# Kernel optimization log

Measured on AMD Instinct MI355X. Metric: run time of the kernel, lower is better.

Reference implementation:

```python
import jax, jax.numpy as jnp
import numpy as np

N = 50000      # nodes
E = 640000     # edges
F_IN = 128     # input features
H = 128        # hidden = 2**7
C = 40         # classes


def setup_inputs() -> dict:
    key = jax.random.key(0)
    ks = jax.random.split(key, 10)
    x = jax.random.normal(ks[0], (N, F_IN), dtype=jnp.float32)
    edge_index = jax.random.randint(ks[1], (2, E), 0, N, dtype=jnp.int32)
    edge_weight = jax.random.uniform(ks[2], (E,), dtype=jnp.float32)
    def glorot(k, fan_in, fan_out):
        s = (6.0 / (fan_in + fan_out)) ** 0.5
        return jax.random.uniform(k, (fan_in, fan_out), jnp.float32, -s, s)
    return {
        "x": x,
        "edge_index": edge_index,
        "edge_weight": edge_weight,
        "W1": glorot(ks[3], F_IN, H), "b1": jnp.zeros((H,), jnp.float32),
        "W2": glorot(ks[4], H, H),    "b2": jnp.zeros((H,), jnp.float32),
        "W3": glorot(ks[5], H, C),    "b3": jnp.zeros((C,), jnp.float32),
    }


def gcn_conv(x, W, b, src, dst, ew, n):
    """PyG GCNConv: add self-loops, symmetric deg normalization, gather-scatter-add."""
    loop = jnp.arange(n, dtype=src.dtype)
    src_sl = jnp.concatenate([src, loop])
    dst_sl = jnp.concatenate([dst, loop])
    w_sl = jnp.concatenate([ew, jnp.ones((n,), ew.dtype)])
    deg = jax.ops.segment_sum(w_sl, dst_sl, num_segments=n)         # [N]
    dinv = jnp.where(deg > 0, jax.lax.rsqrt(deg), 0.0)
    norm = dinv[src_sl] * w_sl * dinv[dst_sl]                        # [E+N]
    h = x @ W                                                        # [N, out]
    msg = h[src_sl] * norm[:, None]                                  # gather + scale
    out = jax.ops.segment_sum(msg, dst_sl, num_segments=n)          # scatter-add
    return out + b


def reference(x, edge_index, edge_weight, W1, b1, W2, b2, W3, b3):
    # eval-mode forward: dropout and dropedge are identity (training=False)
    src, dst = edge_index[0], edge_index[1]
    n = x.shape[0]
    h = jax.nn.relu(gcn_conv(x, W1, b1, src, dst, edge_weight, n))
    h = jax.nn.relu(gcn_conv(h, W2, b2, src, dst, edge_weight, n))
    return gcn_conv(h, W3, b3, src, dst, edge_weight, n)
```

## Files before the change

### kernel.cpp

```cpp
#include <hip/hip_runtime.h>
#include <hip/hip_fp16.h>

constexpr int N_NODES = 50000;
constexpr int N_EDGES = 640000;

constexpr int NBLK  = 256;
constexpr int EPB   = N_EDGES / NBLK;
constexpr int NBUCK = (N_NODES + 255) / 256;
constexpr int GBM   = (N_NODES + 63) / 64;

typedef _Float16 half8  __attribute__((ext_vector_type(8)));
typedef _Float16 half4v __attribute__((ext_vector_type(4)));
typedef float    floatx4 __attribute__((ext_vector_type(4)));


__global__ void wconv_k(const float* __restrict__ W1, const float* __restrict__ W2,
                        const float* __restrict__ W3, _Float16* __restrict__ Wt1,
                        _Float16* __restrict__ Wt2, _Float16* __restrict__ Wt3,
                        float* __restrict__ deg) {
    int i = blockIdx.x * 256 + threadIdx.x;
    if (i < N_NODES) deg[i] = 0.f;
    if (i < 16384) {
        int n = i >> 7, k = i & 127;
        Wt1[n * 128 + k] = (_Float16)W1[k * 128 + n];
    } else if (i < 32768) {
        int j = i - 16384; int n = j >> 7, k = j & 127;
        Wt2[n * 128 + k] = (_Float16)W2[k * 128 + n];
    } else if (i < 32768 + 6144) {
        int j = i - 32768; int n = j >> 7, k = j & 127;
        Wt3[n * 128 + k] = (_Float16)((n < 40) ? W3[k * 40 + n] : 0.f);
    }
}


template<typename TIN, int F_OUT, int NT, bool FUSE_HIST>
__global__ __launch_bounds__(256) void gemm_mfma_k(const TIN* __restrict__ X,
        const _Float16* __restrict__ Wt, __half* __restrict__ H,
        const int* __restrict__ dst, int* __restrict__ gh,
        const float* __restrict__ ew, float* __restrict__ deg) {
    if constexpr (FUSE_HIST) {
        if (blockIdx.x < NBLK) {
            __shared__ int lh[256];
            int t = threadIdx.x, b = blockIdx.x;
            lh[t] = 0;
            __syncthreads();
            int e0 = b * EPB;
            for (int j = t; j < EPB; j += 256) {
                int d = dst[e0 + j];
                atomicAdd(&lh[d >> 8], 1);
                atomicAdd(&deg[d], ew[e0 + j]);
            }
            __syncthreads();
            if (t < NBUCK) gh[b * NBUCK + t] = lh[t];
            return;
        }
    }
    int bid = FUSE_HIST ? (int)blockIdx.x - NBLK : (int)blockIdx.x;

    __shared__ _Float16 Xs[64 * 136];
    int tid = threadIdx.x;
    int row0 = bid * 64;

    if constexpr (sizeof(TIN) == 4) {
        for (int idx = tid; idx < 2048; idx += 256) {
            int r = idx >> 5, c4 = idx & 31;
            float4 v = {0.f, 0.f, 0.f, 0.f};
            if (row0 + r < N_NODES)
                v = *(const float4*)((const float*)X + (size_t)(row0 + r) * 128 + c4 * 4);
            half4v h;
            h[0] = (_Float16)v.x; h[1] = (_Float16)v.y;
            h[2] = (_Float16)v.z; h[3] = (_Float16)v.w;
            *(half4v*)&Xs[r * 136 + c4 * 4] = h;
        }
    } else {
        for (int idx = tid; idx < 1024; idx += 256) {
            int r = idx >> 4, c8 = idx & 15;
            int4 v = {0, 0, 0, 0};
            if (row0 + r < N_NODES)
                v = *(const int4*)((const __half*)X + (size_t)(row0 + r) * 128 + c8 * 8);
            *(int4*)&Xs[r * 136 + c8 * 8] = v;
        }
    }
    __syncthreads();

    int lane = tid & 63;
    int wv   = tid >> 6;
    int m    = lane & 15;
    int q    = lane >> 4;

    half8 af[4];
    #pragma unroll
    for (int kt = 0; kt < 4; kt++)
        af[kt] = *(const half8*)&Xs[(wv * 16 + m) * 136 + kt * 32 + q * 8];

    floatx4 acc[NT];
    #pragma unroll
    for (int nt = 0; nt < NT; nt++) { acc[nt][0] = 0.f; acc[nt][1] = 0.f; acc[nt][2] = 0.f; acc[nt][3] = 0.f; }

    #pragma unroll
    for (int nt = 0; nt < NT; nt++) {
        const _Float16* wp = Wt + (size_t)(nt * 16 + m) * 128 + q * 8;
        half8 b0 = *(const half8*)(wp);
        half8 b1 = *(const half8*)(wp + 32);
        half8 b2 = *(const half8*)(wp + 64);
        half8 b3 = *(const half8*)(wp + 96);
        acc[nt] = __builtin_amdgcn_mfma_f32_16x16x32_f16(af[0], b0, acc[nt], 0, 0, 0);
        acc[nt] = __builtin_amdgcn_mfma_f32_16x16x32_f16(af[1], b1, acc[nt], 0, 0, 0);
        acc[nt] = __builtin_amdgcn_mfma_f32_16x16x32_f16(af[2], b2, acc[nt], 0, 0, 0);
        acc[nt] = __builtin_amdgcn_mfma_f32_16x16x32_f16(af[3], b3, acc[nt], 0, 0, 0);
    }

    #pragma unroll
    for (int nt = 0; nt < NT; nt++) {
        #pragma unroll
        for (int r = 0; r < 4; r++)
            Xs[(wv * 16 + q * 4 + r) * 136 + nt * 16 + m] = (_Float16)acc[nt][r];
    }

    if constexpr (F_OUT == 128) {
        for (int g = lane; g < 256; g += 64) {
            int r = g >> 4, c8 = g & 15;
            int row = row0 + wv * 16 + r;
            if (row < N_NODES)
                *(int4*)((__half*)H + (size_t)row * 128 + c8 * 8) =
                    *(const int4*)&Xs[(wv * 16 + r) * 136 + c8 * 8];
        }
    } else {
        for (int g = lane; g < 80; g += 64) {
            int r = g / 5, seg = g - r * 5;
            int row = row0 + wv * 16 + r;
            if (row < N_NODES)
                *(int4*)((__half*)H + (size_t)row * 40 + seg * 8) =
                    *(const int4*)&Xs[(wv * 16 + r) * 136 + seg * 8];
        }
    }
}


__global__ __launch_bounds__(256) void scan1_k(int* __restrict__ gh, int* __restrict__ total,
                                               const float* __restrict__ deg,
                                               float* __restrict__ dinv) {
    __shared__ int s[256];
    int t = threadIdx.x, b = blockIdx.x;
    int nd = b * 256 + t;
    if (nd < N_NODES) dinv[nd] = rsqrtf(1.0f + deg[nd]);
    int v = gh[t * NBUCK + b];
    s[t] = v;
    __syncthreads();
    int x = v;
    for (int off = 1; off < 256; off <<= 1) {
        int u = (t >= off) ? s[t - off] : 0;
        __syncthreads();
        x += u; s[t] = x;
        __syncthreads();
    }
    gh[t * NBUCK + b] = x - v;
    if (t == 255) total[b] = x;
}


__global__ __launch_bounds__(256) void bucket_k(const int* __restrict__ src,
        const int* __restrict__ dst, const float* __restrict__ ew,
        const int* __restrict__ gh, const int* __restrict__ total,
        int2* __restrict__ bkt) {
    __shared__ int cur[256];
    __shared__ int sc[256];
    int t = threadIdx.x, b = blockIdx.x;
    int v = (t < NBUCK) ? total[t] : 0;
    sc[t] = v;
    __syncthreads();
    int x = v;
    for (int off = 1; off < 256; off <<= 1) {
        int u = (t >= off) ? sc[t - off] : 0;
        __syncthreads();
        x += u; sc[t] = x;
        __syncthreads();
    }
    if (t < NBUCK) cur[t] = (x - v) + gh[b * NBUCK + t];
    __syncthreads();
    int e0 = b * EPB;
    for (int j = t; j < EPB; j += 256) {
        int d = dst[e0 + j];
        int pos = atomicAdd(&cur[d >> 8], 1);
        bkt[pos] = make_int2(src[e0 + j] | (d << 16), __float_as_int(ew[e0 + j]));
    }
}


__global__ __launch_bounds__(256) void final_k(const int2* __restrict__ bkt,
        const int* __restrict__ total, const float* __restrict__ dinv,
        int2* __restrict__ ev, int* __restrict__ rowptr) {
    __shared__ int   cnt[256];
    __shared__ int   s[256];
    __shared__ float dloc[256];
    int t = threadIdx.x, b = blockIdx.x;

    int nd = b * 256 + t;
    dloc[t] = (nd < N_NODES) ? dinv[nd] : 0.f;
    cnt[t] = 0;

    int v = (t < NBUCK) ? total[t] : 0;
    s[t] = v;
    __syncthreads();
    int x = v;
    for (int off = 1; off < 256; off <<= 1) {
        int u = (t >= off) ? s[t - off] : 0;
        __syncthreads();
        x += u; s[t] = x;
        __syncthreads();
    }
    int base = (b == 0) ? 0 : s[b - 1];
    int cntb = total[b];
    __syncthreads();

    for (int j = t; j < cntb; j += 256)
        atomicAdd(&cnt[(bkt[base + j].x >> 16) & 255], 1);
    __syncthreads();

    int v2 = cnt[t];
    s[t] = v2;
    __syncthreads();
    int x2 = v2;
    for (int off = 1; off < 256; off <<= 1) {
        int u = (t >= off) ? s[t - off] : 0;
        __syncthreads();
        x2 += u; s[t] = x2;
        __syncthreads();
    }
    int off_t = x2 - v2;
    if (nd < N_NODES) rowptr[nd] = base + off_t;
    if (b == 0 && t == 0) rowptr[N_NODES] = N_EDGES;
    s[t] = off_t;
    __syncthreads();

    for (int j = t; j < cntb; j += 256) {
        int2 r = bkt[base + j];
        int bin  = (r.x >> 16) & 255;
        int sidx = r.x & 0xFFFF;
        float wv = __int_as_float(r.y) * dinv[sidx] * dloc[bin];
        int p = atomicAdd(&s[bin], 1);
        ev[base + p] = make_int2(sidx, __float_as_int(wv));
    }
}


__global__ __launch_bounds__(256) void agg128_k(const __half* __restrict__ H,
        const int2* __restrict__ ev, const int* __restrict__ rowptr,
        const float* __restrict__ dinv, const float* __restrict__ bias,
        __half* __restrict__ out) {
    int lane = threadIdx.x & 63;
    int node = __builtin_amdgcn_readfirstlane(blockIdx.x * 4 + (threadIdx.x >> 6));
    if (node >= N_NODES) return;
    const __half2* __restrict__ H2 = (const __half2*)H;
    float di = dinv[node];
    float dii = di * di;
    float2 hs = __half22float2(H2[(size_t)node * 64 + lane]);
    float ax = dii * hs.x, ay = dii * hs.y;
    int e0 = rowptr[node], e1 = rowptr[node + 1];
    int e = e0;
    for (; e + 4 <= e1; e += 4) {
        int2 p0 = ev[e + 0];
        int2 p1 = ev[e + 1];
        int2 p2 = ev[e + 2];
        int2 p3 = ev[e + 3];
        float2 g0 = __half22float2(H2[(size_t)p0.x * 64 + lane]);
        float2 g1 = __half22float2(H2[(size_t)p1.x * 64 + lane]);
        float2 g2 = __half22float2(H2[(size_t)p2.x * 64 + lane]);
        float2 g3 = __half22float2(H2[(size_t)p3.x * 64 + lane]);
        float v0 = __int_as_float(p0.y);
        float v1 = __int_as_float(p1.y);
        float v2 = __int_as_float(p2.y);
        float v3 = __int_as_float(p3.y);
        ax = fmaf(v0, g0.x, ax); ay = fmaf(v0, g0.y, ay);
        ax = fmaf(v1, g1.x, ax); ay = fmaf(v1, g1.y, ay);
        ax = fmaf(v2, g2.x, ax); ay = fmaf(v2, g2.y, ay);
        ax = fmaf(v3, g3.x, ax); ay = fmaf(v3, g3.y, ay);
    }
    for (; e < e1; e++) {
        int2 p = ev[e];
        float v = __int_as_float(p.y);
        float2 g = __half22float2(H2[(size_t)p.x * 64 + lane]);
        ax = fmaf(v, g.x, ax);
        ay = fmaf(v, g.y, ay);
    }
    float2 b = *(const float2*)&bias[2 * lane];
    ax = fmaxf(ax + b.x, 0.f);
    ay = fmaxf(ay + b.y, 0.f);
    ((__half2*)out)[(size_t)node * 64 + lane] = __float22half2_rn(make_float2(ax, ay));
}


__global__ __launch_bounds__(256) void agg40_k(const __half* __restrict__ Y,
        const int2* __restrict__ ev, const int* __restrict__ rowptr,
        const float* __restrict__ dinv, const float* __restrict__ bias,
        float* __restrict__ out) {
    int lane = threadIdx.x & 63;
    int node = __builtin_amdgcn_readfirstlane(blockIdx.x * 4 + (threadIdx.x >> 6));
    if (node >= N_NODES) return;
    const __half2* __restrict__ Y2 = (const __half2*)Y;
    int h = lane >> 5;
    int l = lane & 31;
    int f = (l < 20) ? l : 0;
    float di = dinv[node];
    float dii = di * di;
    float ax = 0.f, ay = 0.f;
    if (h == 0) {
        float2 ys = __half22float2(Y2[(size_t)node * 20 + f]);
        ax = dii * ys.x; ay = dii * ys.y;
    }
    int e0 = rowptr[node], e1 = rowptr[node + 1];
    int e = e0;
    for (; e + 4 <= e1; e += 4) {
        int2 p0 = ev[e + h * 2 + 0];
        int2 p1 = ev[e + h * 2 + 1];
        float2 g0 = __half22float2(Y2[(size_t)p0.x * 20 + f]);
        float2 g1 = __half22float2(Y2[(size_t)p1.x * 20 + f]);
        float v0 = __int_as_float(p0.y);
        float v1 = __int_as_float(p1.y);
        ax = fmaf(v0, g0.x, ax); ay = fmaf(v0, g0.y, ay);
        ax = fmaf(v1, g1.x, ax); ay = fmaf(v1, g1.y, ay);
    }
    for (int ee = e + h; ee < e1; ee += 2) {
        int2 p = ev[ee];
        float v = __int_as_float(p.y);
        float2 g = __half22float2(Y2[(size_t)p.x * 20 + f]);
        ax = fmaf(v, g.x, ax);
        ay = fmaf(v, g.y, ay);
    }
    ax += __shfl_xor(ax, 32);
    ay += __shfl_xor(ay, 32);
    if (lane < 20) {
        float2 b = *(const float2*)&bias[2 * lane];
        float2 o;
        o.x = ax + b.x;
        o.y = ay + b.y;
        *(float2*)&out[(size_t)node * 40 + 2 * lane] = o;
    }
}


extern "C" void kernel_launch(void* const* d_in, const int* in_sizes, int n_in,
                              void* d_out, int out_size, void* d_ws, size_t ws_size,
                              hipStream_t stream) {
    const float* x  = (const float*)d_in[0];
    const int*   ei = (const int*)d_in[1];
    const int*   src = ei;
    const int*   dst = ei + N_EDGES;
    const float* ew = (const float*)d_in[2];
    const float* W1 = (const float*)d_in[3];
    const float* b1 = (const float*)d_in[4];
    const float* W2 = (const float*)d_in[5];
    const float* b2 = (const float*)d_in[6];
    const float* W3 = (const float*)d_in[7];
    const float* b3 = (const float*)d_in[8];
    float* out = (float*)d_out;

    char* w = (char*)d_ws;
    auto alloc = [&](size_t bytes) {
        char* p = w;
        w += (bytes + 255) & ~(size_t)255;
        return p;
    };
    float*     dinv   = (float*)    alloc((size_t)N_NODES * 4);
    float*     deg    = (float*)    alloc((size_t)N_NODES * 4);
    int*       rowptr = (int*)      alloc((size_t)(N_NODES + 1) * 4);
    int*       gh     = (int*)      alloc((size_t)NBLK * NBUCK * 4);
    int*       total  = (int*)      alloc((size_t)NBUCK * 4);
    int2*      bkt    = (int2*)     alloc((size_t)N_EDGES * 8);
    int2*      ev     = (int2*)     alloc((size_t)N_EDGES * 8);
    __half*    hbuf   = (__half*)   alloc((size_t)N_NODES * 128 * 2);
    __half*    abuf   = (__half*)   alloc((size_t)N_NODES * 128 * 2);
    __half*    ybuf   = (__half*)   alloc((size_t)N_NODES * 40 * 2);
    _Float16*  Wt1    = (_Float16*) alloc((size_t)128 * 128 * 2);
    _Float16*  Wt2    = (_Float16*) alloc((size_t)128 * 128 * 2);
    _Float16*  Wt3    = (_Float16*) alloc((size_t)48 * 128 * 2);

    constexpr int GA = (N_NODES + 3) / 4;

    wconv_k<<<196, 256, 0, stream>>>(W1, W2, W3, Wt1, Wt2, Wt3, deg);
    gemm_mfma_k<float, 128, 8, true><<<NBLK + GBM, 256, 0, stream>>>(x, Wt1, hbuf, dst, gh, ew, deg);
    scan1_k<<<NBUCK, 256, 0, stream>>>(gh, total, deg, dinv);
    bucket_k<<<NBLK, 256, 0, stream>>>(src, dst, ew, gh, total, bkt);
    final_k<<<NBUCK, 256, 0, stream>>>(bkt, total, dinv, ev, rowptr);

    agg128_k<<<GA, 256, 0, stream>>>(hbuf, ev, rowptr, dinv, b1, abuf);
    gemm_mfma_k<__half, 128, 8, false><<<GBM, 256, 0, stream>>>(abuf, Wt2, hbuf, nullptr, nullptr, nullptr, nullptr);
    agg128_k<<<GA, 256, 0, stream>>>(hbuf, ev, rowptr, dinv, b2, abuf);
    gemm_mfma_k<__half, 40, 3, false><<<GBM, 256, 0, stream>>>(abuf, Wt3, ybuf, nullptr, nullptr, nullptr, nullptr);
    agg40_k<<<GA, 256, 0, stream>>>(ybuf, ev, rowptr, dinv, b3, out);
}
```

Measured before the change: 268.8 us.

## Compute degrees in final_k and defer source-side normalization to first aggregation

Degree accumulation moves out of the histogram pass, which used global float atomics on deg, and into final_k as per-bucket shared-memory atomic sums, which also write dinv. Because dinv of source nodes is not yet known when final_k writes edge values, the first 128-wide aggregation multiplies each edge weight by dinv[src] and writes the normalized value back into ev for later layers. This removes global atomics and the deg buffer and its zeroing. In exchange, the first aggregation pays extra dinv gathers and scattered writes to ev.

Measured after the change: 257.0 us. 1.05x faster.

```diff
diff --git a/kernel.cpp b/kernel.cpp
--- a/kernel.cpp
+++ b/kernel.cpp
@@ -16,10 +16,8 @@
 
 __global__ void wconv_k(const float* __restrict__ W1, const float* __restrict__ W2,
                         const float* __restrict__ W3, _Float16* __restrict__ Wt1,
-                        _Float16* __restrict__ Wt2, _Float16* __restrict__ Wt3,
-                        float* __restrict__ deg) {
+                        _Float16* __restrict__ Wt2, _Float16* __restrict__ Wt3) {
     int i = blockIdx.x * 256 + threadIdx.x;
-    if (i < N_NODES) deg[i] = 0.f;
     if (i < 16384) {
         int n = i >> 7, k = i & 127;
         Wt1[n * 128 + k] = (_Float16)W1[k * 128 + n];
@@ -36,8 +34,7 @@
 template<typename TIN, int F_OUT, int NT, bool FUSE_HIST>
 __global__ __launch_bounds__(256) void gemm_mfma_k(const TIN* __restrict__ X,
         const _Float16* __restrict__ Wt, __half* __restrict__ H,
-        const int* __restrict__ dst, int* __restrict__ gh,
-        const float* __restrict__ ew, float* __restrict__ deg) {
+        const int* __restrict__ dst, int* __restrict__ gh) {
     if constexpr (FUSE_HIST) {
         if (blockIdx.x < NBLK) {
             __shared__ int lh[256];
@@ -45,11 +42,8 @@
             lh[t] = 0;
             __syncthreads();
             int e0 = b * EPB;
-            for (int j = t; j < EPB; j += 256) {
-                int d = dst[e0 + j];
-                atomicAdd(&lh[d >> 8], 1);
-                atomicAdd(&deg[d], ew[e0 + j]);
-            }
+            for (int j = t; j < EPB; j += 256)
+                atomicAdd(&lh[dst[e0 + j] >> 8], 1);
             __syncthreads();
             if (t < NBUCK) gh[b * NBUCK + t] = lh[t];
             return;
@@ -137,13 +131,9 @@
 }
 
 
-__global__ __launch_bounds__(256) void scan1_k(int* __restrict__ gh, int* __restrict__ total,
-                                               const float* __restrict__ deg,
-                                               float* __restrict__ dinv) {
+__global__ __launch_bounds__(256) void scan1_k(int* __restrict__ gh, int* __restrict__ total) {
     __shared__ int s[256];
     int t = threadIdx.x, b = blockIdx.x;
-    int nd = b * 256 + t;
-    if (nd < N_NODES) dinv[nd] = rsqrtf(1.0f + deg[nd]);
     int v = gh[t * NBUCK + b];
     s[t] = v;
     __syncthreads();
@@ -188,16 +178,14 @@
 
 
 __global__ __launch_bounds__(256) void final_k(const int2* __restrict__ bkt,
-        const int* __restrict__ total, const float* __restrict__ dinv,
-        int2* __restrict__ ev, int* __restrict__ rowptr) {
+        const int* __restrict__ total, int2* __restrict__ ev,
+        int* __restrict__ rowptr, float* __restrict__ dinv) {
     __shared__ int   cnt[256];
+    __shared__ float wsum[256];
     __shared__ int   s[256];
-    __shared__ float dloc[256];
     int t = threadIdx.x, b = blockIdx.x;
 
-    int nd = b * 256 + t;
-    dloc[t] = (nd < N_NODES) ? dinv[nd] : 0.f;
-    cnt[t] = 0;
+    cnt[t] = 0; wsum[t] = 0.f;
 
     int v = (t < NBUCK) ? total[t] : 0;
     s[t] = v;
@@ -213,8 +201,12 @@
     int cntb = total[b];
     __syncthreads();
 
-    for (int j = t; j < cntb; j += 256)
-        atomicAdd(&cnt[(bkt[base + j].x >> 16) & 255], 1);
+    for (int j = t; j < cntb; j += 256) {
+        int2 r = bkt[base + j];
+        int bin = (r.x >> 16) & 255;
+        atomicAdd(&cnt[bin], 1);
+        atomicAdd(&wsum[bin], __int_as_float(r.y));
+    }
     __syncthreads();
 
     int v2 = cnt[t];
@@ -228,8 +220,14 @@
         __syncthreads();
     }
     int off_t = x2 - v2;
-    if (nd < N_NODES) rowptr[nd] = base + off_t;
+    int nd = b * 256 + t;
+    float dv = rsqrtf(1.0f + wsum[t]);
+    if (nd < N_NODES) {
+        rowptr[nd] = base + off_t;
+        dinv[nd]   = dv;
+    }
     if (b == 0 && t == 0) rowptr[N_NODES] = N_EDGES;
+    wsum[t] = dv;
     s[t] = off_t;
     __syncthreads();
 
@@ -237,15 +235,16 @@
         int2 r = bkt[base + j];
         int bin  = (r.x >> 16) & 255;
         int sidx = r.x & 0xFFFF;
-        float wv = __int_as_float(r.y) * dinv[sidx] * dloc[bin];
+        float wv = __int_as_float(r.y) * wsum[bin];
         int p = atomicAdd(&s[bin], 1);
         ev[base + p] = make_int2(sidx, __float_as_int(wv));
     }
 }
 
 
+template<bool PREMUL>
 __global__ __launch_bounds__(256) void agg128_k(const __half* __restrict__ H,
-        const int2* __restrict__ ev, const int* __restrict__ rowptr,
+        int2* __restrict__ ev, const int* __restrict__ rowptr,
         const float* __restrict__ dinv, const float* __restrict__ bias,
         __half* __restrict__ out) {
     int lane = threadIdx.x & 63;
@@ -263,14 +262,24 @@
         int2 p1 = ev[e + 1];
         int2 p2 = ev[e + 2];
         int2 p3 = ev[e + 3];
+        float v0 = __int_as_float(p0.y);
+        float v1 = __int_as_float(p1.y);
+        float v2 = __int_as_float(p2.y);
+        float v3 = __int_as_float(p3.y);
+        if constexpr (PREMUL) {
+            v0 *= dinv[p0.x]; v1 *= dinv[p1.x];
+            v2 *= dinv[p2.x]; v3 *= dinv[p3.x];
+            if (lane == 0) {
+                ev[e + 0].y = __float_as_int(v0);
+                ev[e + 1].y = __float_as_int(v1);
+                ev[e + 2].y = __float_as_int(v2);
+                ev[e + 3].y = __float_as_int(v3);
+            }
+        }
         float2 g0 = __half22float2(H2[(size_t)p0.x * 64 + lane]);
         float2 g1 = __half22float2(H2[(size_t)p1.x * 64 + lane]);
         float2 g2 = __half22float2(H2[(size_t)p2.x * 64 + lane]);
         float2 g3 = __half22float2(H2[(size_t)p3.x * 64 + lane]);
-        float v0 = __int_as_float(p0.y);
-        float v1 = __int_as_float(p1.y);
-        float v2 = __int_as_float(p2.y);
-        float v3 = __int_as_float(p3.y);
         ax = fmaf(v0, g0.x, ax); ay = fmaf(v0, g0.y, ay);
         ax = fmaf(v1, g1.x, ax); ay = fmaf(v1, g1.y, ay);
         ax = fmaf(v2, g2.x, ax); ay = fmaf(v2, g2.y, ay);
@@ -279,6 +288,10 @@
     for (; e < e1; e++) {
         int2 p = ev[e];
         float v = __int_as_float(p.y);
+        if constexpr (PREMUL) {
+            v *= dinv[p.x];
+            if (lane == 0) ev[e].y = __float_as_int(v);
+        }
         float2 g = __half22float2(H2[(size_t)p.x * 64 + lane]);
         ax = fmaf(v, g.x, ax);
         ay = fmaf(v, g.y, ay);
@@ -362,7 +375,6 @@
         return p;
     };
     float*     dinv   = (float*)    alloc((size_t)N_NODES * 4);
-    float*     deg    = (float*)    alloc((size_t)N_NODES * 4);
     int*       rowptr = (int*)      alloc((size_t)(N_NODES + 1) * 4);
     int*       gh     = (int*)      alloc((size_t)NBLK * NBUCK * 4);
     int*       total  = (int*)      alloc((size_t)NBUCK * 4);
@@ -377,15 +389,15 @@
 
     constexpr int GA = (N_NODES + 3) / 4;
 
-    wconv_k<<<196, 256, 0, stream>>>(W1, W2, W3, Wt1, Wt2, Wt3, deg);
-    gemm_mfma_k<float, 128, 8, true><<<NBLK + GBM, 256, 0, stream>>>(x, Wt1, hbuf, dst, gh, ew, deg);
-    scan1_k<<<NBUCK, 256, 0, stream>>>(gh, total, deg, dinv);
+    wconv_k<<<152, 256, 0, stream>>>(W1, W2, W3, Wt1, Wt2, Wt3);
+    gemm_mfma_k<float, 128, 8, true><<<NBLK + GBM, 256, 0, stream>>>(x, Wt1, hbuf, dst, gh);
+    scan1_k<<<NBUCK, 256, 0, stream>>>(gh, total);
     bucket_k<<<NBLK, 256, 0, stream>>>(src, dst, ew, gh, total, bkt);
-    final_k<<<NBUCK, 256, 0, stream>>>(bkt, total, dinv, ev, rowptr);
-
-    agg128_k<<<GA, 256, 0, stream>>>(hbuf, ev, rowptr, dinv, b1, abuf);
-    gemm_mfma_k<__half, 128, 8, false><<<GBM, 256, 0, stream>>>(abuf, Wt2, hbuf, nullptr, nullptr, nullptr, nullptr);
-    agg128_k<<<GA, 256, 0, stream>>>(hbuf, ev, rowptr, dinv, b2, abuf);
-    gemm_mfma_k<__half, 40, 3, false><<<GBM, 256, 0, stream>>>(abuf, Wt3, ybuf, nullptr, nullptr, nullptr, nullptr);
+    final_k<<<NBUCK, 256, 0, stream>>>(bkt, total, ev, rowptr, dinv);
+
+    agg128_k<true ><<<GA, 256, 0, stream>>>(hbuf, ev, rowptr, dinv, b1, abuf);
+    gemm_mfma_k<__half, 128, 8, false><<<GBM, 256, 0, stream>>>(abuf, Wt2, hbuf, nullptr, nullptr);
+    agg128_k<false><<<GA, 256, 0, stream>>>(hbuf, ev, rowptr, dinv, b2, abuf);
+    gemm_mfma_k<__half, 40, 3, false><<<GBM, 256, 0, stream>>>(abuf, Wt3, ybuf, nullptr, nullptr);
     agg40_k<<<GA, 256, 0, stream>>>(ybuf, ev, rowptr, dinv, b3, out);
 }
```
